# Optimization experiments

Hardware: AMD Instinct MI355X
Metric: run time of the kernel (lower is better)

## Reference

```python
import jax, jax.numpy as jnp
import numpy as np

N_NODES = 10242  # icosphere level-5 node count
NNZ = 71694      # ~7 nonzeros per row (6 neighbors + self)


def setup_inputs() -> dict:
    key = jax.random.key(0)
    k1, k2, k3, k4, k5 = jax.random.split(key, 5)
    B, T, C, Cout, Ks = 2, 16, 16, 32, 20
    x = jax.random.normal(k1, (B, T, N_NODES, C), dtype=jnp.float32)
    edge_row = jax.random.randint(k2, (NNZ,), 0, N_NODES, dtype=jnp.int32)
    edge_col = jax.random.randint(k3, (NNZ,), 0, N_NODES, dtype=jnp.int32)
    # small values keep the Chebyshev recurrence numerically bounded over Ks steps
    edge_val = jax.random.uniform(k4, (NNZ,), dtype=jnp.float32, minval=-0.2, maxval=0.2)
    W = jax.random.normal(k5, (Cout, C * Ks), dtype=jnp.float32) * 0.02
    return {"x": x, "edge_row": edge_row, "edge_col": edge_col,
            "edge_val": edge_val, "W": W}


def reference(x, edge_row, edge_col, edge_val, W):
    B, T, N, C = x.shape
    Cout, CK = W.shape
    Ks = CK // C

    def spmm(v):  # sparse L @ v, v: [N, F]
        return jax.ops.segment_sum(edge_val[:, None] * v[edge_col], edge_row,
                                   num_segments=N)

    # [B,T,N,C] -> [B*T,N,C] -> [N,C,B*T] -> [N, C*B*T]
    x0 = x.reshape(B * T, N, C).transpose(1, 2, 0).reshape(N, C * B * T)
    x1 = spmm(x0)

    def step(carry, _):
        a, b = carry
        c = 2.0 * spmm(b) - a
        return (b, c), c

    _, rest = jax.lax.scan(step, (x0, x1), None, length=Ks - 2)
    xs = jnp.concatenate([x0[None], x1[None], rest], axis=0)  # [Ks, N, C*B*T]

    xs = xs.reshape(Ks, N, C, B * T).transpose(3, 1, 2, 0)  # [B*T, N, C, Ks]
    xs = xs.reshape(B * T * N, C * Ks)
    out = xs @ W.T  # [B*T*N, Cout]
    return out.reshape(B, T, N, Cout)
```

## Files before the change

### kernel.cpp

```cpp
#include <hip/hip_runtime.h>

#define N_NODES 10242
#define NNZ_E   71694
#define NNZ_PAD_MAX (NNZ_E + 7 * N_NODES + 64)
#define BT      32
#define C_IN    16
#define K_S     20
#define C_OUT   32
#define F       512
typedef unsigned short u16;
typedef unsigned int   u32;
typedef unsigned long long u64;

#define RING_ELEMS ((size_t)N_NODES * F)
#define RING_BYTES (RING_ELEMS * 2)

#define OVFL_FLAG (1 << 30)

typedef __attribute__((ext_vector_type(8)))  _Float16 half8;
typedef __attribute__((ext_vector_type(16))) float    float16;

__device__ __forceinline__ void unpack8h(uint4 u, float* f) {
    union { uint4 u; _Float16 h[8]; } v; v.u = u;
    #pragma unroll
    for (int i = 0; i < 8; ++i) f[i] = (float)v.h[i];
}
__device__ __forceinline__ uint4 pack8h(const float* f) {
    union { uint4 u; _Float16 h[8]; } v;
    #pragma unroll
    for (int i = 0; i < 8; ++i) v.h[i] = (_Float16)f[i];
    return v.u;
}
__device__ __forceinline__ u16 f2h(float f) {
    union { _Float16 h; u16 u; } v; v.h = (_Float16)f; return v.u;
}


__global__ __launch_bounds__(256) void init_kernel(
        const float* __restrict__ W, int* __restrict__ cnt,
        u16* __restrict__ wtfrag) {
    int i = blockIdx.x * 256 + threadIdx.x;
    if (i < N_NODES) cnt[i] = 0;
    int w = i - N_NODES;
    if (w >= 0 && w < K_S * 64 * 8) {
        int j    = w & 7;
        int lane = (w >> 3) & 63;
        int k    = w >> 9;
        int cout = lane & 31;
        int c    = ((lane >> 5) << 3) + j;
        wtfrag[w] = f2h(W[cout * (C_IN * K_S) + c * K_S + k]);
    }
}

__global__ __launch_bounds__(256) void count_kernel(
        const int* __restrict__ erow, int* cnt) {
    int e = blockIdx.x * 256 + threadIdx.x;
    if (e < NNZ_E) atomicAdd(&cnt[erow[e]], 1);
}

__global__ __launch_bounds__(256) void scan_kernel(
        const int* __restrict__ cnt, int* row_ptr, int* cursor) {
    const int T = 256;
    const int chunk = (N_NODES + T - 1) / T;
    __shared__ int part[T];
    int t = threadIdx.x;
    int base = t * chunk;
    int s = 0;
    for (int i = 0; i < chunk; ++i) {
        int idx = base + i;
        if (idx < N_NODES) s += (cnt[idx] + 7) & ~7;
    }
    part[t] = s;
    __syncthreads();
    for (int off = 1; off < T; off <<= 1) {
        int v = (t >= off) ? part[t - off] : 0;
        __syncthreads();
        part[t] += v;
        __syncthreads();
    }
    int run = (t == 0) ? 0 : part[t - 1];
    for (int i = 0; i < chunk; ++i) {
        int idx = base + i;
        if (idx < N_NODES) {
            row_ptr[idx] = run;
            cursor[idx]  = run;
            run += (cnt[idx] + 7) & ~7;
        }
    }
    if (t == T - 1) row_ptr[N_NODES] = part[T - 1];
}

__global__ __launch_bounds__(256) void scatter_kernel(
        const int* __restrict__ erow, const int* __restrict__ ecol,
        const float* __restrict__ eval, int* cursor, int2* __restrict__ cpack) {
    int e = blockIdx.x * 256 + threadIdx.x;
    if (e < NNZ_E) {
        int p = atomicAdd(&cursor[erow[e]], 1);
        cpack[p] = make_int2(ecol[e], __float_as_int(eval[e]));
    }
}

__global__ __launch_bounds__(256) void finalize_kernel(
        const int* __restrict__ row_ptr, const int* __restrict__ cursor,
        int2* cpack, int2* __restrict__ epk16) {
    const int lane = threadIdx.x & 63;
    const int r = (blockIdx.x << 2) + (threadIdx.x >> 6);
    if (r >= N_NODES) return;
    const int sbeg = row_ptr[r];
    const int send = cursor[r];
    const int pend = row_ptr[r + 1];
    const int rlen = send - sbeg;
    const int plen = pend - sbeg;

    if (plen > 64) {
        if (lane == 0) {
            for (int i = sbeg + 1; i < send; ++i) {
                int2 key = cpack[i];
                int j = i - 1;
                while (j >= sbeg) {
                    int2 q = cpack[j];
                    bool gt = (q.x > key.x) || (q.x == key.x && (u32)q.y > (u32)key.y);
                    if (!gt) break;
                    cpack[j + 1] = q; --j;
                }
                cpack[j + 1] = key;
            }
            for (int p = send; p < pend; ++p) cpack[p] = make_int2(0, 0);
            for (int p = 0; p < 16; ++p) {
                int2 v = (p < plen) ? cpack[sbeg + p] : make_int2(0, 0);
                if (p == 15 && rlen > 16) v.x |= OVFL_FLAG;
                epk16[(size_t)r * 16 + p] = v;
            }
        }
        return;
    }

    const bool real = (lane < rlen);
    int2 e = real ? cpack[sbeg + lane] : make_int2(0, 0);
    const u64 ki = ((u64)(u32)e.x << 32) | (u32)e.y;

    int rank = 0;
    for (int j = 0; j < rlen; ++j) {
        int cx = __shfl(e.x, j, 64);
        int cy = __shfl(e.y, j, 64);
        u64 kj = ((u64)(u32)cx << 32) | (u32)cy;
        if (kj < ki || (kj == ki && j < lane)) ++rank;
    }
    if (!real) rank = lane;

    if (lane < plen) cpack[sbeg + rank] = real ? e : make_int2(0, 0);

    int2 v16 = real ? e : make_int2(0, 0);
    if (rank == 15 && rlen > 16) v16.x |= OVFL_FLAG;
    if (rank < 16) epk16[(size_t)r * 16 + rank] = v16;
}


__global__ __launch_bounds__(256) void transform_kernel(
        const float* __restrict__ x, u16* __restrict__ T0) {
    int g = blockIdx.x * 256 + threadIdx.x;
    int n   = g >> 9;
    int rem = g & 511;
    int bt  = rem >> 4;
    int c   = rem & 15;
    float v = x[((size_t)bt * N_NODES + n) * C_IN + c];
    T0[(size_t)n * F + rem] = f2h(v);
}


__global__ __launch_bounds__(256) void spmm16_kernel(
        const u16* __restrict__ srcB, const u16* __restrict__ srcA,
        u16* __restrict__ dst,
        const int2* __restrict__ epk16,
        const int* __restrict__ row_ptr, const int2* __restrict__ cpack,
        float alpha, float beta) {
    const int lane = threadIdx.x & 63;
    const int n = (blockIdx.x << 2) + (threadIdx.x >> 6);
    if (n >= N_NODES) return;

    int2 my = epk16[(size_t)n * 16 + (lane & 15)];
    float a[8] = {0,0,0,0,0,0,0,0};
    if (beta != 0.f) {
        uint4 ua = ((const uint4*)(srcA + (size_t)n * F))[lane];
        unpack8h(ua, a);
    }

    int   c[16]; float v[16];
    #pragma unroll
    for (int r = 0; r < 16; ++r) {
        c[r] = __builtin_amdgcn_readlane(my.x, r) & 0xFFFF;
        v[r] = __int_as_float(__builtin_amdgcn_readlane(my.y, r));
    }

    uint4 g[16];
    #pragma unroll
    for (int r = 0; r < 16; ++r)
        g[r] = ((const uint4*)(srcB + (size_t)c[r] * F))[lane];

    float acc0[8] = {0,0,0,0,0,0,0,0};
    float acc1[8] = {0,0,0,0,0,0,0,0};
    #pragma unroll
    for (int r = 0; r < 16; r += 2) {
        float b0[8], b1[8];
        unpack8h(g[r], b0);
        unpack8h(g[r + 1], b1);
        #pragma unroll
        for (int i = 0; i < 8; ++i) {
            acc0[i] += v[r]     * b0[i];
            acc1[i] += v[r + 1] * b1[i];
        }
    }

    if (__builtin_amdgcn_readlane(my.x, 15) & OVFL_FLAG) {
        int s = row_ptr[n], e_end = row_ptr[n + 1];
        for (int e = s + 16; e < e_end; e += 8) {
            int2 m2 = cpack[e + (lane & 7)];
            #pragma unroll
            for (int r = 0; r < 8; ++r) {
                int   cc = __builtin_amdgcn_readlane(m2.x, r);
                float vv = __int_as_float(__builtin_amdgcn_readlane(m2.y, r));
                uint4 gg = ((const uint4*)(srcB + (size_t)cc * F))[lane];
                float bb[8];
                unpack8h(gg, bb);
                #pragma unroll
                for (int i = 0; i < 8; ++i) acc0[i] += vv * bb[i];
            }
        }
    }

    float y[8];
    #pragma unroll
    for (int i = 0; i < 8; ++i)
        y[i] = alpha * (acc0[i] + acc1[i]) + beta * a[i];

    ((uint4*)(dst + (size_t)n * F))[lane] = pack8h(y);
}


__global__ __launch_bounds__(256) void proj_mfma_kernel(
        const u16* __restrict__ ring, int R, int k0, int kcnt,
        const u16* __restrict__ wtfrag, float* __restrict__ out, int accumulate) {
    const int lane = threadIdx.x & 63;
    const int n = (blockIdx.x << 2) + (threadIdx.x >> 6);
    if (n >= N_NODES) return;
    const int col = lane & 31;
    const int grp = lane >> 5;
    const size_t aoff = (size_t)n * F + (size_t)col * 16 + grp * 8;

    union U { uint4 u; half8 h; };
    float16 acc0 = {};
    float16 acc1 = {};
    int j = 0;
    for (; j + 2 <= kcnt; j += 2) {
        int ka = k0 + j, kb = k0 + j + 1;
        U a0, b0, a1, b1;
        a0.u = *(const uint4*)(ring + (size_t)(ka % R) * RING_ELEMS + aoff);
        b0.u = *(const uint4*)(wtfrag + (size_t)ka * 512 + lane * 8);
        a1.u = *(const uint4*)(ring + (size_t)(kb % R) * RING_ELEMS + aoff);
        b1.u = *(const uint4*)(wtfrag + (size_t)kb * 512 + lane * 8);
        acc0 = __builtin_amdgcn_mfma_f32_32x32x16_f16(a0.h, b0.h, acc0, 0, 0, 0);
        acc1 = __builtin_amdgcn_mfma_f32_32x32x16_f16(a1.h, b1.h, acc1, 0, 0, 0);
    }
    if (j < kcnt) {
        int ka = k0 + j;
        U a0, b0;
        a0.u = *(const uint4*)(ring + (size_t)(ka % R) * RING_ELEMS + aoff);
        b0.u = *(const uint4*)(wtfrag + (size_t)ka * 512 + lane * 8);
        acc0 = __builtin_amdgcn_mfma_f32_32x32x16_f16(a0.h, b0.h, acc0, 0, 0, 0);
    }

    #pragma unroll
    for (int r = 0; r < 16; ++r) {
        int bt = (r & 3) + 8 * (r >> 2) + 4 * grp;
        float* op = out + ((size_t)bt * N_NODES + n) * C_OUT + col;
        float val = acc0[r] + acc1[r];
        if (accumulate) *op += val;
        else            *op  = val;
    }
}


extern "C" void kernel_launch(void* const* d_in, const int* in_sizes, int n_in,
                              void* d_out, int out_size, void* d_ws, size_t ws_size,
                              hipStream_t stream) {
    const float* x    = (const float*)d_in[0];
    const int*   erow = (const int*)  d_in[1];
    const int*   ecol = (const int*)  d_in[2];
    const float* eval = (const float*)d_in[3];
    const float* W    = (const float*)d_in[4];
    float* out = (float*)d_out;

    char* ws = (char*)d_ws;
    size_t o = 0;
    auto alloc = [&](size_t bytes) -> char* {
        o = (o + 511) & ~(size_t)511;
        char* r = ws + o;
        o += bytes;
        return r;
    };
    int*   cnt     = (int*)  alloc((size_t)N_NODES * 4);
    int*   row_ptr = (int*)  alloc((size_t)(N_NODES + 1) * 4);
    int*   cursor  = (int*)  alloc((size_t)N_NODES * 4);
    int2*  cpack   = (int2*) alloc((size_t)NNZ_PAD_MAX * 8);
    int2*  epk16   = (int2*) alloc((size_t)N_NODES * 16 * 8);
    u16*   wtfrag  = (u16*)  alloc((size_t)K_S * 512 * 2);

    o = (o + 511) & ~(size_t)511;
    int R = (int)((ws_size - o) / RING_BYTES);
    if (R > K_S) R = K_S;
    if (R < 3)  R = 3;
    u16* ring = (u16*)(ws + o);
    auto slot = [&](int k) -> u16* { return ring + (size_t)(k % R) * RING_ELEMS; };

    init_kernel<<<(N_NODES + K_S * 512 + 255) / 256, 256, 0, stream>>>(W, cnt, wtfrag);
    count_kernel<<<(NNZ_E + 255) / 256, 256, 0, stream>>>(erow, cnt);
    scan_kernel<<<1, 256, 0, stream>>>(cnt, row_ptr, cursor);
    scatter_kernel<<<(NNZ_E + 255) / 256, 256, 0, stream>>>(erow, ecol, eval, cursor, cpack);
    finalize_kernel<<<(N_NODES + 3) / 4, 256, 0, stream>>>(row_ptr, cursor, cpack, epk16);

    const int grid4 = (N_NODES + 3) / 4;
    int c0 = 0;
    auto maybe_pass = [&](int k_done) {
        int target = K_S - c0;
        if (target > R) target = R;
        if (target > 0 && (k_done - c0 + 1) == target) {
            proj_mfma_kernel<<<grid4, 256, 0, stream>>>(
                ring, R, c0, target, wtfrag, out, (c0 > 0) ? 1 : 0);
            c0 += target;
        }
    };

    transform_kernel<<<(int)(RING_ELEMS / 256), 256, 0, stream>>>(x, slot(0));
    maybe_pass(0);

    for (int k = 1; k < K_S; ++k) {
        const u16* srcB = slot(k - 1);
        const u16* srcA = (k >= 2) ? slot(k - 2) : slot(k - 1);
        float alpha = (k == 1) ? 1.f : 2.f;
        float beta  = (k == 1) ? 0.f : -1.f;
        spmm16_kernel<<<grid4, 256, 0, stream>>>(
            srcB, srcA, slot(k), epk16, row_ptr, cpack, alpha, beta);
        maybe_pass(k);
    }
}
```

Baseline: 420.0 us.

## Fuse Chebyshev recurrence into one cooperative persistent kernel with per-XCC barriers

Replaces the 19 separate spmm launches plus the transform launch with a single cooperative persistent kernel of 256 blocks. Each block discovers its XCC and splits the feature dimension by XCC, 64 features per die. Blocks synchronise only within their XCC through a counter barrier, so each die's L2 keeps its slice of the ring. Loads use sc0 inline asm so data written by other CUs is seen, and all K_S terms then go to one projection pass. The cost is a dependence on cooperative launch support, spin-wait overhead, and an assumption of 8 XCCs each holding a balanced share of blocks.

```diff
diff --git a/kernel.cpp b/kernel.cpp
--- a/kernel.cpp
+++ b/kernel.cpp
@@ -1,4 +1,7 @@
 #include <hip/hip_runtime.h>
+#include <hip/hip_cooperative_groups.h>
+
+namespace cg = cooperative_groups;
 
 #define N_NODES 10242
 #define NNZ_E   71694
@@ -35,12 +38,51 @@
     union { _Float16 h; u16 u; } v; v.h = (_Float16)f; return v.u;
 }
 
+__device__ __forceinline__ uint4 ld16_sc0(const u16* p) {
+    uint4 q;
+    asm volatile("global_load_dwordx4 %0, %1, off sc0\n\t"
+                 "s_waitcnt vmcnt(0)"
+                 : "=&v"(q) : "v"(p) : "memory");
+    __builtin_amdgcn_sched_barrier(0);
+    return q;
+}
+__device__ __forceinline__ void g8_sc0(const u16* sB, size_t lo2,
+        int c0, int c1, int c2, int c3, int c4, int c5, int c6, int c7,
+        uint4& q0, uint4& q1, uint4& q2, uint4& q3,
+        uint4& q4, uint4& q5, uint4& q6, uint4& q7) {
+    const u16* p0 = sB + (size_t)c0 * F + lo2;
+    const u16* p1 = sB + (size_t)c1 * F + lo2;
+    const u16* p2 = sB + (size_t)c2 * F + lo2;
+    const u16* p3 = sB + (size_t)c3 * F + lo2;
+    const u16* p4 = sB + (size_t)c4 * F + lo2;
+    const u16* p5 = sB + (size_t)c5 * F + lo2;
+    const u16* p6 = sB + (size_t)c6 * F + lo2;
+    const u16* p7 = sB + (size_t)c7 * F + lo2;
+    asm volatile(
+        "global_load_dwordx4 %0, %8,  off sc0\n\t"
+        "global_load_dwordx4 %1, %9,  off sc0\n\t"
+        "global_load_dwordx4 %2, %10, off sc0\n\t"
+        "global_load_dwordx4 %3, %11, off sc0\n\t"
+        "global_load_dwordx4 %4, %12, off sc0\n\t"
+        "global_load_dwordx4 %5, %13, off sc0\n\t"
+        "global_load_dwordx4 %6, %14, off sc0\n\t"
+        "global_load_dwordx4 %7, %15, off sc0\n\t"
+        "s_waitcnt vmcnt(0)"
+        : "=&v"(q0), "=&v"(q1), "=&v"(q2), "=&v"(q3),
+          "=&v"(q4), "=&v"(q5), "=&v"(q6), "=&v"(q7)
+        : "v"(p0), "v"(p1), "v"(p2), "v"(p3),
+          "v"(p4), "v"(p5), "v"(p6), "v"(p7)
+        : "memory");
+    __builtin_amdgcn_sched_barrier(0);
+}
+
 
 __global__ __launch_bounds__(256) void init_kernel(
         const float* __restrict__ W, int* __restrict__ cnt,
-        u16* __restrict__ wtfrag) {
+        u16* __restrict__ wtfrag, int* __restrict__ syncp) {
     int i = blockIdx.x * 256 + threadIdx.x;
     if (i < N_NODES) cnt[i] = 0;
+    if (i < 16) syncp[i] = 0;
     int w = i - N_NODES;
     if (w >= 0 && w < K_S * 64 * 8) {
         int j    = w & 7;
@@ -156,6 +198,169 @@
 }
 
 
+__device__ __forceinline__ void xbar(int* sync, int xcc, int nb, int target_mult) {
+    asm volatile("s_waitcnt vmcnt(0)" ::: "memory");
+    __syncthreads();
+    if (threadIdx.x == 0) {
+        __hip_atomic_fetch_add(&sync[8 + xcc], 1, __ATOMIC_RELAXED,
+                               __HIP_MEMORY_SCOPE_AGENT);
+        const int tgt = target_mult * nb;
+        while (__hip_atomic_load(&sync[8 + xcc], __ATOMIC_RELAXED,
+                                 __HIP_MEMORY_SCOPE_AGENT) < tgt)
+            __builtin_amdgcn_s_sleep(16);
+    }
+    __syncthreads();
+    asm volatile("" ::: "memory");
+}
+
+
+__global__ __launch_bounds__(1024) void chain_bsp_kernel(
+        const float* __restrict__ x,
+        const int* __restrict__ row_ptr, const int2* __restrict__ cpack,
+        const int2* __restrict__ epk16,
+        u16* __restrict__ ring, int* __restrict__ sync) {
+    __shared__ int shv[2];
+    __shared__ char lds_force[81920];
+    cg::grid_group grid = cg::this_grid();
+
+    if (threadIdx.x == 0) {
+        ((volatile char*)lds_force)[0] = 0;
+        int xcc = __builtin_amdgcn_s_getreg((31 << 11) | (0 << 6) | 20) & 7;
+        shv[0] = xcc;
+        shv[1] = atomicAdd(&sync[xcc], 1);
+    }
+    __syncthreads();
+    const int xcc  = shv[0];
+    const int rank = shv[1];
+    grid.sync();
+    const int nb = sync[xcc];
+
+    const int w     = threadIdx.x >> 6;
+    const int l     = threadIdx.x & 63;
+    const int g     = l >> 3;
+    const int gl    = l & 7;
+    const int gbase = l & 56;
+    const int f0    = xcc << 6;
+
+    const int chunk = (N_NODES + nb - 1) / nb;
+    const int n0 = rank * chunk;
+    int n1 = n0 + chunk; if (n1 > N_NODES) n1 = N_NODES;
+
+    for (int n8 = n0 + w * 8; n8 < n1; n8 += 128) {
+        int n = n8 + g;
+        if (n < n1) {
+            int f = f0 + gl * 8;
+            const float* xp = x + ((size_t)(f >> 4) * N_NODES + n) * C_IN + (f & 15);
+            float4 u0 = *(const float4*)xp;
+            float4 u1 = *(const float4*)(xp + 4);
+            float t0v[8] = {u0.x, u0.y, u0.z, u0.w, u1.x, u1.y, u1.z, u1.w};
+            *(uint4*)(ring + (size_t)n * F + f) = pack8h(t0v);
+        }
+    }
+    xbar(sync, xcc, nb, 1);
+
+    for (int k = 1; k < K_S; ++k) {
+        const u16* sB = ring + (size_t)(k - 1) * RING_ELEMS;
+        const u16* sA = ring + (size_t)((k >= 2) ? k - 2 : 0) * RING_ELEMS;
+        u16*       dp = ring + (size_t)k * RING_ELEMS;
+        const float alpha = (k == 1) ? 1.f : 2.f;
+        const bool hasA = (k >= 2);
+        const size_t lo2 = (size_t)f0 + (size_t)gl * 8;
+
+        for (int n8 = n0 + w * 8; n8 < n1; n8 += 128) {
+            int n = n8 + g;
+            if (n >= n1) continue;
+            const size_t nlo = (size_t)n * F + lo2;
+
+            float a[8] = {0,0,0,0,0,0,0,0};
+            if (hasA) { uint4 ua = ld16_sc0(sA + nlo); unpack8h(ua, a); }
+
+            int4 m4 = ((const int4*)(epk16 + (size_t)n * 16))[gl];
+            int plen = row_ptr[n + 1] - row_ptr[n];
+
+            float acc[8] = {0,0,0,0,0,0,0,0};
+            {
+                int cc[8]; float vv[8];
+                #pragma unroll
+                for (int r = 0; r < 8; ++r) {
+                    int src = gbase + (r >> 1);
+                    int cx = __shfl((r & 1) ? m4.z : m4.x, src, 64);
+                    int vy = __shfl((r & 1) ? m4.w : m4.y, src, 64);
+                    cc[r] = cx & 0xFFFF;
+                    vv[r] = __int_as_float(vy);
+                }
+                uint4 q0,q1,q2,q3,q4,q5,q6,q7;
+                g8_sc0(sB, lo2, cc[0],cc[1],cc[2],cc[3],cc[4],cc[5],cc[6],cc[7],
+                       q0,q1,q2,q3,q4,q5,q6,q7);
+                float b[8];
+                unpack8h(q0,b); for(int i=0;i<8;++i) acc[i]+=vv[0]*b[i];
+                unpack8h(q1,b); for(int i=0;i<8;++i) acc[i]+=vv[1]*b[i];
+                unpack8h(q2,b); for(int i=0;i<8;++i) acc[i]+=vv[2]*b[i];
+                unpack8h(q3,b); for(int i=0;i<8;++i) acc[i]+=vv[3]*b[i];
+                unpack8h(q4,b); for(int i=0;i<8;++i) acc[i]+=vv[4]*b[i];
+                unpack8h(q5,b); for(int i=0;i<8;++i) acc[i]+=vv[5]*b[i];
+                unpack8h(q6,b); for(int i=0;i<8;++i) acc[i]+=vv[6]*b[i];
+                unpack8h(q7,b); for(int i=0;i<8;++i) acc[i]+=vv[7]*b[i];
+            }
+            if (plen > 8) {
+                int cc[8]; float vv[8];
+                #pragma unroll
+                for (int r = 0; r < 8; ++r) {
+                    int src = gbase + 4 + (r >> 1);
+                    int cx = __shfl((r & 1) ? m4.z : m4.x, src, 64);
+                    int vy = __shfl((r & 1) ? m4.w : m4.y, src, 64);
+                    cc[r] = cx & 0xFFFF;
+                    vv[r] = __int_as_float(vy);
+                }
+                uint4 q0,q1,q2,q3,q4,q5,q6,q7;
+                g8_sc0(sB, lo2, cc[0],cc[1],cc[2],cc[3],cc[4],cc[5],cc[6],cc[7],
+                       q0,q1,q2,q3,q4,q5,q6,q7);
+                float b[8];
+                unpack8h(q0,b); for(int i=0;i<8;++i) acc[i]+=vv[0]*b[i];
+                unpack8h(q1,b); for(int i=0;i<8;++i) acc[i]+=vv[1]*b[i];
+                unpack8h(q2,b); for(int i=0;i<8;++i) acc[i]+=vv[2]*b[i];
+                unpack8h(q3,b); for(int i=0;i<8;++i) acc[i]+=vv[3]*b[i];
+                unpack8h(q4,b); for(int i=0;i<8;++i) acc[i]+=vv[4]*b[i];
+                unpack8h(q5,b); for(int i=0;i<8;++i) acc[i]+=vv[5]*b[i];
+                unpack8h(q6,b); for(int i=0;i<8;++i) acc[i]+=vv[6]*b[i];
+                unpack8h(q7,b); for(int i=0;i<8;++i) acc[i]+=vv[7]*b[i];
+            }
+            if (plen > 16) {
+                int s = row_ptr[n];
+                for (int base = 16; base < plen; base += 8) {
+                    int2 m2 = cpack[s + base + gl];
+                    int cc[8]; float vv[8];
+                    #pragma unroll
+                    for (int r = 0; r < 8; ++r) {
+                        cc[r] = __shfl(m2.x, gbase + r, 64) & 0xFFFF;
+                        vv[r] = __int_as_float(__shfl(m2.y, gbase + r, 64));
+                    }
+                    uint4 q0,q1,q2,q3,q4,q5,q6,q7;
+                    g8_sc0(sB, lo2, cc[0],cc[1],cc[2],cc[3],cc[4],cc[5],cc[6],cc[7],
+                           q0,q1,q2,q3,q4,q5,q6,q7);
+                    float b[8];
+                    unpack8h(q0,b); for(int i=0;i<8;++i) acc[i]+=vv[0]*b[i];
+                    unpack8h(q1,b); for(int i=0;i<8;++i) acc[i]+=vv[1]*b[i];
+                    unpack8h(q2,b); for(int i=0;i<8;++i) acc[i]+=vv[2]*b[i];
+                    unpack8h(q3,b); for(int i=0;i<8;++i) acc[i]+=vv[3]*b[i];
+                    unpack8h(q4,b); for(int i=0;i<8;++i) acc[i]+=vv[4]*b[i];
+                    unpack8h(q5,b); for(int i=0;i<8;++i) acc[i]+=vv[5]*b[i];
+                    unpack8h(q6,b); for(int i=0;i<8;++i) acc[i]+=vv[6]*b[i];
+                    unpack8h(q7,b); for(int i=0;i<8;++i) acc[i]+=vv[7]*b[i];
+                }
+            }
+
+            float y[8];
+            #pragma unroll
+            for (int i = 0; i < 8; ++i)
+                y[i] = alpha * acc[i] - (hasA ? a[i] : 0.f);
+            *(uint4*)(dp + nlo) = pack8h(y);
+        }
+        if (k < K_S - 1) xbar(sync, xcc, nb, k + 1);
+    }
+}
+
+
 __global__ __launch_bounds__(256) void transform_kernel(
         const float* __restrict__ x, u16* __restrict__ T0) {
     int g = blockIdx.x * 256 + threadIdx.x;
@@ -166,7 +371,6 @@
     float v = x[((size_t)bt * N_NODES + n) * C_IN + c];
     T0[(size_t)n * F + rem] = f2h(v);
 }
-
 
 __global__ __launch_bounds__(256) void spmm16_kernel(
         const u16* __restrict__ srcB, const u16* __restrict__ srcA,
@@ -304,6 +508,7 @@
     int2*  cpack   = (int2*) alloc((size_t)NNZ_PAD_MAX * 8);
     int2*  epk16   = (int2*) alloc((size_t)N_NODES * 16 * 8);
     u16*   wtfrag  = (u16*)  alloc((size_t)K_S * 512 * 2);
+    int*   syncp   = (int*)  alloc(16 * 4);
 
     o = (o + 511) & ~(size_t)511;
     int R = (int)((ws_size - o) / RING_BYTES);
@@ -312,13 +517,29 @@
     u16* ring = (u16*)(ws + o);
     auto slot = [&](int k) -> u16* { return ring + (size_t)(k % R) * RING_ELEMS; };
 
-    init_kernel<<<(N_NODES + K_S * 512 + 255) / 256, 256, 0, stream>>>(W, cnt, wtfrag);
+    init_kernel<<<(N_NODES + K_S * 512 + 255) / 256, 256, 0, stream>>>(W, cnt, wtfrag, syncp);
     count_kernel<<<(NNZ_E + 255) / 256, 256, 0, stream>>>(erow, cnt);
     scan_kernel<<<1, 256, 0, stream>>>(cnt, row_ptr, cursor);
     scatter_kernel<<<(NNZ_E + 255) / 256, 256, 0, stream>>>(erow, ecol, eval, cursor, cpack);
     finalize_kernel<<<(N_NODES + 3) / 4, 256, 0, stream>>>(row_ptr, cursor, cpack, epk16);
 
     const int grid4 = (N_NODES + 3) / 4;
+
+    if (R >= K_S) {
+        const float* xa = x; const int* rpa = row_ptr; const int2* cpa = cpack;
+        const int2* eka = epk16; u16* ra = ring; int* sy = syncp;
+        void* args[] = {(void*)&xa, (void*)&rpa, (void*)&cpa,
+                        (void*)&eka, (void*)&ra, (void*)&sy};
+        hipError_t err = hipLaunchCooperativeKernel(
+            (const void*)chain_bsp_kernel, dim3(256), dim3(1024), args, 0, stream);
+        if (err == hipSuccess) {
+            proj_mfma_kernel<<<grid4, 256, 0, stream>>>(
+                ring, K_S, 0, K_S, wtfrag, out, 0);
+            return;
+        }
+        (void)hipGetLastError();
+    }
+
     int c0 = 0;
     auto maybe_pass = [&](int k_done) {
         int target = K_S - c0;
@@ -332,7 +553,6 @@
 
     transform_kernel<<<(int)(RING_ELEMS / 256), 256, 0, stream>>>(x, slot(0));
     maybe_pass(0);
-
     for (int k = 1; k < K_S; ++k) {
         const u16* srcB = slot(k - 1);
         const u16* srcA = (k >= 2) ? slot(k - 2) : slot(k - 1);
```

After: 494.7 us. 1.18x slower.
